# Kernel optimization log

Measured on AMD Instinct MI355X. Metric: run time of the kernel, lower is better.

Reference implementation:

```python
import jax, jax.numpy as jnp
import numpy as np

B, L, D, NH, NITEMS = 256, 200, 128, 2, 100000
HD = D // NH
LAMB = 0.6
NEG = -1e9

_PARAM_SHAPES = dict(
    item_emb=(NITEMS, D), pos_emb=(L, D),
    W_ei=(D, D), b_ei=(D,), W_eo=(D, D), b_eo=(D,), b_iah=(D,), b_oah=(D,),
    w_ih=(3 * D, 2 * D), b_ih=(3 * D,), w_hh=(3 * D, D), b_hh=(3 * D,),
    ln1_g=(D,), ln1_b=(D,),
    Wq=(D, D), bq=(D,), Wk=(D, D), bk=(D,), Wv=(D, D), bv=(D,), Wo=(D, D), bo=(D,),
    ln2_g=(D,), ln2_b=(D,), W1=(D, D), b1=(D,), W2=(D, D), b2=(D,),
    lnf_g=(D,), lnf_b=(D,),
)


def setup_inputs() -> dict:
    key = jax.random.key(0)
    ks = jax.random.split(key, len(_PARAM_SHAPES) + 2)
    stdv = 1.0 / np.sqrt(D)  # GCSAN._init_weights: uniform(-stdv, stdv) on ALL params
    p = {}
    for i, (name, shp) in enumerate(_PARAM_SHAPES.items()):
        p[name] = jax.random.uniform(ks[i], shp, jnp.float32, -stdv, stdv)
    lens = jax.random.randint(ks[-2], (B,), L // 4, L + 1)
    vals = jax.random.randint(ks[-1], (B, L), 1, NITEMS)
    # trailing zero padding, as the original break-on-zero loop assumes
    seqs = jnp.where(jnp.arange(L)[None, :] < lens[:, None], vals, 0).astype(jnp.int32)
    p['seqs'] = seqs
    p['lens'] = lens.astype(jnp.int32)
    return p


def _ln(x, g, b):
    mu = x.mean(-1, keepdims=True)
    var = ((x - mu) ** 2).mean(-1, keepdims=True)
    return (x - mu) / jnp.sqrt(var + 1e-5) * g + b


def _build_graph(seqs):
    # Vectorized replacement of _get_slice (per-row np.unique + adjacency build)
    def per_row(seq):
        s = jnp.sort(seq)
        first = jnp.concatenate([jnp.ones((1,), bool), s[1:] != s[:-1]])
        pos = jnp.cumsum(first) - 1  # compaction target of each first-occurrence
        items = jnp.zeros((L,), seq.dtype).at[jnp.where(first, pos, L)].set(s, mode='drop')
        n_u = first.sum()
        search = jnp.where(jnp.arange(L) < n_u, items, jnp.iinfo(jnp.int32).max)
        alias = jnp.searchsorted(search, seq).astype(jnp.int32)
        return items, alias
    items, alias = jax.vmap(per_row)(seqs)
    valid = seqs[:, 1:] > 0  # edge (i -> i+1) exists until first pad
    u = jnp.where(valid, alias[:, :-1], L)  # route masked edges to dummy row L
    v = jnp.where(valid, alias[:, 1:], L)
    bidx = jnp.arange(B)[:, None]
    uA = jnp.zeros((B, L + 1, L + 1), jnp.float32).at[bidx, u, v].set(1.0)[:, :L, :L]
    in_deg = jnp.maximum(uA.sum(1), 1.0)
    out_deg = jnp.maximum(uA.sum(2), 1.0)
    A_in = jnp.swapaxes(uA, 1, 2) / in_deg[:, :, None]   # A[i,j] = uA[j,i]/in_deg[i]
    A_out = uA / out_deg[:, :, None]                     # A[i,k] = uA[i,k]/out_deg[i]
    return alias, jnp.concatenate([A_in, A_out], axis=2), items  # A: [B, L, 2L]


def reference(item_emb, pos_emb, W_ei, b_ei, W_eo, b_eo, b_iah, b_oah,
              w_ih, b_ih, w_hh, b_hh, ln1_g, ln1_b, Wq, bq, Wk, bk, Wv, bv,
              Wo, bo, ln2_g, ln2_b, W1, b1, W2, b2, lnf_g, lnf_b, seqs, lens):
    alias, A, items = _build_graph(seqs)
    hidden = item_emb[items]  # [B, L, D]
    # SR-GNN gated cell, step = n_layers = 1
    for _ in range(1):
        h_in = jnp.einsum('bij,bjd->bid', A[:, :, :L], hidden @ W_ei.T + b_ei) + b_iah
        h_out = jnp.einsum('bij,bjd->bid', A[:, :, L:], hidden @ W_eo.T + b_eo) + b_oah
        gi = jnp.concatenate([h_in, h_out], -1) @ w_ih.T + b_ih
        gh = hidden @ w_hh.T + b_hh
        i_r, i_i, i_n = jnp.split(gi, 3, -1)
        h_r, h_i, h_n = jnp.split(gh, 3, -1)
        r = jax.nn.sigmoid(i_r + h_r)
        z = jax.nn.sigmoid(i_i + h_i)
        ng = jnp.tanh(i_n + r * h_n)
        hidden = ng + z * (hidden - ng)
    bidx = jnp.arange(B)
    seq_hidden = hidden[bidx[:, None], alias]  # alias-gather back to sequence order
    last_idx = lens - 1
    ht = seq_hidden[bidx, last_idx]
    x = seq_hidden + pos_emb[None, :, :]
    tl_mask = (seqs > 0)[:, :, None].astype(x.dtype)
    x = x * tl_mask
    causal = jnp.triu(jnp.ones((L, L), bool), 1)  # True = masked future (bidirectional=False)
    # SASRec-style block: ln -> MHA residual -> ln -> pointwise FFN residual
    q_in = _ln(x, ln1_g, ln1_b)
    heads = lambda t: t.reshape(B, L, NH, HD).transpose(0, 2, 1, 3)
    q = heads(q_in @ Wq.T + bq)
    k = heads(x @ Wk.T + bk)
    v = heads(x @ Wv.T + bv)
    sc = jnp.einsum('bhqd,bhkd->bhqk', q, k) / jnp.sqrt(jnp.asarray(HD, x.dtype))
    sc = jnp.where(causal[None, None], NEG, sc)
    attn = jax.nn.softmax(sc, -1)
    mo = jnp.einsum('bhqk,bhkd->bhqd', attn, v).transpose(0, 2, 1, 3).reshape(B, L, D) @ Wo.T + bo
    x = q_in + mo
    h = _ln(x, ln2_g, ln2_b)
    x = h + jax.nn.relu(h @ W1.T + b1) @ W2.T + b2
    x = x * tl_mask
    log_feats = _ln(x, lnf_g, lnf_b)
    out = log_feats[bidx, last_idx]
    return LAMB * out + (1.0 - LAMB) * ht
```

## Files before the change

### kernel.cpp

```cpp
#include <hip/hip_runtime.h>
#include <hip/hip_bf16.h>

#define Bb 256
#define Ll 200
#define Dd 128
#define BL (Bb*Ll)

typedef __hip_bfloat16 bf16;
typedef __attribute__((ext_vector_type(8))) short short8;
typedef __attribute__((ext_vector_type(4))) unsigned short ushort4v;
typedef __attribute__((ext_vector_type(4))) float floatx4;

__device__ __forceinline__ float b2f(bf16 v) { return __bfloat162float(v); }
__device__ __forceinline__ bf16  f2b(float v) { return __float2bfloat16(v); }
__device__ __forceinline__ float us2f(unsigned short u) { return __uint_as_float(((unsigned)u) << 16); }
__device__ __forceinline__ unsigned short f2us(float v) { bf16 t = f2b(v); return *(unsigned short*)&t; }
__device__ __forceinline__ float ldf(const void* p, int i, int f32) {
  return f32 ? ((const float*)p)[i] : b2f(((const bf16*)p)[i]);
}
__device__ __forceinline__ int detect_f32(const unsigned short* __restrict__ w) {
  unsigned short u = w[threadIdx.x & 63];
  return (__ballot(((u >> 7) & 0xFF) >= 0x7F) != 0ull) ? 1 : 0;
}
__device__ __forceinline__ void load_lds16(const void* g, void* l) {
  __builtin_amdgcn_global_load_lds((const __attribute__((address_space(1))) unsigned int*)g,
                                   (__attribute__((address_space(3))) unsigned int*)l, 16, 0, 0);
}

struct PackP {
  const void *W_ei,*W_eo,*w_ih,*w_hh,*Wk,*Wv,*Wqp,*Wop,*W1p,*W2p,*pos;
  const void *b_ei,*b_eo,*b_ih,*b_hh,*bk,*bv,*bqp,*bop,*b1p,*b2p,*biah,*boah;
  const void *ln1g,*ln1b,*ln2g,*ln2b,*lnfg,*lnfb;
  bf16 *cWhe,*cWih,*cWhh,*cWkv,*cWq,*cWo,*cW1,*cW2,*cPos;
  float *bias_he,*bias_gi,*bias_gh,*bias_kv,*cbq,*cbo,*cb1,*cb2,*cbiah,*cboah,*cln;
  const int* seqs;
  int *alias_g, *items_g; float *rin_g, *rout_g; unsigned *adj_g, *adjT_g;
};
__global__ __launch_bounds__(256) void k01(PackP p) {
  __shared__ alignas(16) int s[Ll];
  __shared__ int al[Ll], its[Ll];
  __shared__ alignas(4) unsigned char isf[Ll];
  __shared__ unsigned adjL[Ll*8], adjTL[Ll*8];
  if (blockIdx.x >= Bb) {
    int idx = (blockIdx.x - Bb) * 256 + threadIdx.x;
    int f32 = detect_f32((const unsigned short*)p.W_ei);
    if (idx < 131072) {
      if (idx < 32768) {
        int r = idx >> 7, c = idx & 127;
        p.cWhe[idx] = f2b(r < 128 ? ldf(p.W_ei, r*128+c, f32) : ldf(p.W_eo, (r-128)*128+c, f32));
      } else p.cWih[idx-32768] = f2b(ldf(p.w_ih, idx-32768, f32));
    } else if (idx < 278528) {
      if (idx < 180224)      p.cWhh[idx-131072] = f2b(ldf(p.w_hh, idx-131072, f32));
      else if (idx < 212992) {
        int i = idx - 180224; int r = i >> 7, c = i & 127;
        p.cWkv[i] = f2b(r < 128 ? ldf(p.Wk, r*128+c, f32) : ldf(p.Wv, (r-128)*128+c, f32));
      }
      else if (idx < 229376) p.cWq[idx-212992] = f2b(ldf(p.Wqp, idx-212992, f32));
      else if (idx < 245760) p.cWo[idx-229376] = f2b(ldf(p.Wop, idx-229376, f32));
      else if (idx < 262144) p.cW1[idx-245760] = f2b(ldf(p.W1p, idx-245760, f32));
      else                   p.cW2[idx-262144] = f2b(ldf(p.W2p, idx-262144, f32));
    } else if (idx < 304128) {
      p.cPos[idx-278528] = f2b(ldf(p.pos, idx-278528, f32));
    } else {
      int j = idx - 304128;
      if      (j < 256)  p.bias_he[j]     = (j<128) ? ldf(p.b_ei,j,f32) : ldf(p.b_eo,j-128,f32);
      else if (j < 640)  p.bias_gi[j-256] = ldf(p.b_ih, j-256, f32);
      else if (j < 1024) p.bias_gh[j-640] = ldf(p.b_hh, j-640, f32);
      else if (j < 1280) { int c=j-1024; p.bias_kv[c] = (c<128)? ldf(p.bk,c,f32): ldf(p.bv,c-128,f32); }
      else if (j < 1408) p.cbq[j-1280]   = ldf(p.bqp, j-1280, f32);
      else if (j < 1536) p.cbo[j-1408]   = ldf(p.bop, j-1408, f32);
      else if (j < 1664) p.cb1[j-1536]   = ldf(p.b1p, j-1536, f32);
      else if (j < 1792) p.cb2[j-1664]   = ldf(p.b2p, j-1664, f32);
      else if (j < 1920) p.cbiah[j-1792] = ldf(p.biah, j-1792, f32);
      else if (j < 2048) p.cboah[j-1920] = ldf(p.boah, j-1920, f32);
      else {
        int i = j - 2048, g = i >> 7, c2 = i & 127;
        const void* s6 = g==0?p.ln1g: g==1?p.ln1b: g==2?p.ln2g: g==3?p.ln2b: g==4?p.lnfg: p.lnfb;
        p.cln[i] = ldf(s6, c2, f32);
      }
    }
    return;
  }
  int b = blockIdx.x, t = threadIdx.x;
  if (t < Ll) s[t] = p.seqs[b*Ll + t];
  for (int i = t; i < Ll*8; i += 256) { adjL[i] = 0u; adjTL[i] = 0u; }
  __syncthreads();
  const int4* s4 = (const int4*)s;
  if (t < Ll) {
    int v = s[t]; int dup = 0;
    int nb = t >> 2;
    for (int j4 = 0; j4 < nb; j4++) {
      int4 sv = s4[j4];
      dup |= (sv.x==v) | (sv.y==v) | (sv.z==v) | (sv.w==v);
    }
    for (int j = nb*4; j < t; j++) dup |= (s[j]==v);
    isf[t] = dup ? 0 : 1; its[t] = 0;
  }
  __syncthreads();
  const unsigned* isfw = (const unsigned*)isf;
  if (t < Ll) {
    int v = s[t], r = 0;
    for (int j4 = 0; j4 < Ll/4; j4++) {
      int4 sv = s4[j4];
      unsigned fw = isfw[j4];
      r += ((fw & 0xffu)       && sv.x < v);
      r += ((fw & 0xff00u)     && sv.y < v);
      r += ((fw & 0xff0000u)   && sv.z < v);
      r += ((fw & 0xff000000u) && sv.w < v);
    }
    al[t] = r;
  }
  __syncthreads();
  if (t < Ll && isf[t]) its[al[t]] = s[t];
  if (t < Ll-1 && s[t+1] > 0) {
    int u = al[t], v = al[t+1];
    atomicOr(&adjL [u*8 + (v >> 5)], 1u << (v & 31));
    atomicOr(&adjTL[v*8 + (u >> 5)], 1u << (u & 31));
  }
  __syncthreads();
  if (t < Ll) {
    int od = 0, id = 0;
    for (int wd = 0; wd < 7; wd++) { od += __popc(adjL[t*8+wd]); id += __popc(adjTL[t*8+wd]); }
    p.rout_g [b*Ll + t] = 1.0f / (float)max(od, 1);
    p.rin_g  [b*Ll + t] = 1.0f / (float)max(id, 1);
    p.alias_g[b*Ll + t] = al[t];
    p.items_g[b*Ll + t] = its[t];
  }
  for (int i = t; i < Ll*8; i += 256) { p.adj_g[b*Ll*8 + i] = adjL[i]; p.adjT_g[b*Ll*8 + i] = adjTL[i]; }
}

__global__ __launch_bounds__(256) void k2_gather(const void* __restrict__ emb, const void* __restrict__ wei,
    const int* __restrict__ items_g, bf16* __restrict__ hidden)
{
  int idx = blockIdx.x * 256 + threadIdx.x;
  int f32 = detect_f32((const unsigned short*)wei);
  int n = idx >> 4, jv = idx & 15;
  int it = items_g[n];
  short8 o;
  if (f32) {
    const float* e = (const float*)emb + (size_t)it * 128 + jv * 8;
#pragma unroll
    for (int j = 0; j < 8; j++) o[j] = (short)f2us(e[j]);
  } else {
    o = ((const short8*)((const bf16*)emb + (size_t)it * 128))[jv];
  }
  ((short8*)hidden)[idx] = o;
}

template<int K>
__global__ __launch_bounds__(256) void gemm6(const bf16* __restrict__ A, const bf16* __restrict__ W,
    const float* __restrict__ bias,
    bf16* __restrict__ out_lo, int Nlo, bf16* __restrict__ out_hi, int Nhi, int split)
{
  __shared__ short As[128*128];
  __shared__ short Ws[128*128];
  int t = threadIdx.x;
  int wave = t >> 6, lane = t & 63;
  int q = lane >> 4, mr = lane & 15;
  int wm = wave & 1, wn = wave >> 1;
  int m0 = blockIdx.x * 128, n0 = blockIdx.y * 128;
  int srow = lane >> 4;
  int c16 = lane & 15;
  floatx4 acc[4][4] = {};
  for (int k0 = 0; k0 < K; k0 += 128) {
#pragma unroll
    for (int i = 0; i < 8; i++) {
      int seg = wave*8 + i;
      int r = seg*4 + srow;
      int gch = c16 ^ (r & 15);
      load_lds16(A + (size_t)(m0 + r) * K + k0 + gch*8, &As[seg*512]);
      load_lds16(W + (size_t)(n0 + r) * K + k0 + gch*8, &Ws[seg*512]);
    }
    __syncthreads();
#pragma unroll
    for (int kk = 0; kk < 4; kk++) {
      short8 af[4], wf[4];
#pragma unroll
      for (int i = 0; i < 4; i++) {
        int row = wm*64 + i*16 + mr;
        af[i] = *(const short8*)(&As[row*128 + ((kk*4+q) ^ (row&15))*8]);
      }
#pragma unroll
      for (int j = 0; j < 4; j++) {
        int row = wn*64 + j*16 + mr;
        wf[j] = *(const short8*)(&Ws[row*128 + ((kk*4+q) ^ (row&15))*8]);
      }
#pragma unroll
      for (int i = 0; i < 4; i++)
#pragma unroll
        for (int j = 0; j < 4; j++)
          acc[i][j] = __builtin_amdgcn_mfma_f32_16x16x32_bf16(wf[j], af[i], acc[i][j], 0, 0, 0);
    }
    if (k0 + 128 < K) __syncthreads();
  }
#pragma unroll
  for (int j = 0; j < 4; j++) {
    int ng = n0 + wn*64 + j*16 + q*4;
    floatx4 bs = *(const floatx4*)(bias + ng);
    bf16* outp; int col, stride;
    if (ng < split) { outp = out_lo; col = ng; stride = Nlo; }
    else            { outp = out_hi; col = ng - split; stride = Nhi; }
#pragma unroll
    for (int i = 0; i < 4; i++) {
      int m = m0 + wm*64 + i*16 + mr;
      ushort4v o;
#pragma unroll
      for (int e = 0; e < 4; e++) o[e] = f2us(acc[i][j][e] + bs[e]);
      *(ushort4v*)(outp + (size_t)m * stride + col) = o;
    }
  }
}

__global__ __launch_bounds__(256) void k3_agg(const bf16* __restrict__ he,
    const unsigned* __restrict__ adj_g, const unsigned* __restrict__ adjT_g,
    const float* __restrict__ rin_g, const float* __restrict__ rout_g,
    const float* __restrict__ cbiah, const float* __restrict__ cboah, bf16* __restrict__ hio)
{
  int b = blockIdx.x / 25, chunk = blockIdx.x % 25;
  int wave = threadIdx.x >> 6, lane = threadIdx.x & 63;
  bool isIn = lane < 32;
  int c = isIn ? 4*lane : 128 + 4*(lane-32);
  const bf16* heb = he + (size_t)b * Ll * 256;
  bf16* hiob = hio + (size_t)b * Ll * 256;
  float bias0 = isIn ? cbiah[c]   : cboah[c-128];
  float bias1 = isIn ? cbiah[c+1] : cboah[c-127];
  float bias2 = isIn ? cbiah[c+2] : cboah[c-126];
  float bias3 = isIn ? cbiah[c+3] : cboah[c-125];
#pragma unroll
  for (int s = 0; s < 2; s++) {
    int i = chunk*8 + wave + 4*s;
    const unsigned* mrow = (isIn ? adjT_g : adj_g) + ((size_t)b*Ll + i) * 8;
    float a0=0.f, a1=0.f, a2=0.f, a3=0.f;
    for (int wd = 0; wd < 7; wd++) {
      unsigned bits = mrow[wd];
      while (bits) {
        int j = (wd << 5) + __builtin_ctz(bits); bits &= bits - 1;
        ushort4v h4 = *(const ushort4v*)(heb + (size_t)j*256 + c);
        a0 += us2f(h4.x); a1 += us2f(h4.y); a2 += us2f(h4.z); a3 += us2f(h4.w);
      }
    }
    float r = isIn ? rin_g[b*Ll + i] : rout_g[b*Ll + i];
    ushort4v o;
    o.x = f2us(bias0 + r*a0); o.y = f2us(bias1 + r*a1);
    o.z = f2us(bias2 + r*a2); o.w = f2us(bias3 + r*a3);
    *(ushort4v*)(hiob + (size_t)i*256 + c) = o;
  }
}

__global__ __launch_bounds__(256) void kv_fused(const bf16* __restrict__ gi, const bf16* __restrict__ gh,
    const bf16* __restrict__ hidden, const int* __restrict__ alias_g, const int* __restrict__ lens,
    const bf16* __restrict__ cPos, const bf16* __restrict__ cWkv, const float* __restrict__ bias_kv,
    bf16* __restrict__ kv, float* __restrict__ ht)
{
  __shared__ short xs[208*136];
  __shared__ int aliasL[Ll];
  int b = blockIdx.x, t = threadIdx.x;
  int wave = t >> 6, lane = t & 63, q = lane >> 4, mr = lane & 15;
  int li = lens[b] - 1;
  if (t < Ll) aliasL[t] = alias_g[b*Ll + t];
  for (int u = t; u < 8*136; u += 256) xs[Ll*136 + u] = 0;
  __syncthreads();
  for (int u = t; u < Ll*16; u += 256) {
    int tpos = u >> 4, jv = u & 15;
    int a = aliasL[tpos];
    const short8* gin = (const short8*)(gi + ((size_t)b*Ll + a) * 384);
    const short8* ghn = (const short8*)(gh + ((size_t)b*Ll + a) * 384);
    short8 vir = gin[jv], vii = gin[16+jv], vnn = gin[32+jv];
    short8 whr = ghn[jv], whi = ghn[16+jv], whn = ghn[32+jv];
    short8 hv  = ((const short8*)(hidden + ((size_t)b*Ll + a) * Dd))[jv];
    short8 pv  = ((const short8*)(cPos + tpos * Dd))[jv];
    bool isLast = (tpos == li);
    short8 o;
#pragma unroll
    for (int e = 0; e < 8; e++) {
      float ir = us2f((unsigned short)vir[e]), ii = us2f((unsigned short)vii[e]), inn = us2f((unsigned short)vnn[e]);
      float hr = us2f((unsigned short)whr[e]), hi = us2f((unsigned short)whi[e]), hn = us2f((unsigned short)whn[e]);
      float r  = 1.f / (1.f + __expf(-(ir + hr)));
      float z  = 1.f / (1.f + __expf(-(ii + hi)));
      float arg = inn + r * hn;
      float ex = __expf(-2.f * arg);
      float ng = (1.f - ex) / (1.f + ex);
      float h  = us2f((unsigned short)hv[e]);
      float sh = ng + z * (h - ng);
      o[e] = (short)f2us(sh + us2f((unsigned short)pv[e]));
      if (isLast) ht[b*Dd + jv*8 + e] = sh;
    }
    *(short8*)&xs[tpos*136 + jv*8] = o;
  }
  __syncthreads();
  short8 wf[4][4];
#pragma unroll
  for (int kk = 0; kk < 4; kk++)
#pragma unroll
    for (int j = 0; j < 4; j++) {
      int n = wave*64 + j*16 + mr;
      wf[kk][j] = *(const short8*)(cWkv + (size_t)n*128 + kk*32 + q*8);
    }
  for (int mt = 0; mt < 13; mt++) {
    short8 af[4];
#pragma unroll
    for (int kk = 0; kk < 4; kk++)
      af[kk] = *(const short8*)&xs[(mt*16 + mr)*136 + (kk*4+q)*8];
    floatx4 acc[4] = {};
#pragma unroll
    for (int kk = 0; kk < 4; kk++)
#pragma unroll
      for (int j = 0; j < 4; j++)
        acc[j] = __builtin_amdgcn_mfma_f32_16x16x32_bf16(wf[kk][j], af[kk], acc[j], 0, 0, 0);
    int m = mt*16 + mr;
    if (m < Ll) {
#pragma unroll
      for (int j = 0; j < 4; j++) {
        int n = wave*64 + j*16 + q*4;
        floatx4 bs = *(const floatx4*)(bias_kv + n);
        ushort4v o;
#pragma unroll
        for (int e = 0; e < 4; e++) o[e] = f2us(acc[j][e] + bs[e]);
        *(ushort4v*)(kv + ((size_t)b*Ll + m)*256 + n) = o;
      }
    }
  }
}

struct FinalP {
  const bf16 *kv; const float* ht; const bf16* cPos;
  const bf16 *cWq, *cWo, *cW1, *cW2;
  const float *cbq, *cbo, *cb1, *cb2, *cln;
  const int* lens; const void* wei;
  void* out;
};
__device__ __forceinline__ float dot128i(const bf16* __restrict__ wrow, const float* __restrict__ vin) {
  const short8* wr = (const short8*)wrow;
  float a0=0.f, a1=0.f, a2=0.f, a3=0.f;
#pragma unroll
  for (int kk = 0; kk < 4; kk++) {
    short8 w0 = wr[kk*4+0], w1 = wr[kk*4+1], w2 = wr[kk*4+2], w3 = wr[kk*4+3];
#pragma unroll
    for (int j = 0; j < 8; j++) {
      a0 += vin[kk*32 +      j] * us2f((unsigned short)w0[j]);
      a1 += vin[kk*32 + 8  + j] * us2f((unsigned short)w1[j]);
      a2 += vin[kk*32 + 16 + j] * us2f((unsigned short)w2[j]);
      a3 += vin[kk*32 + 24 + j] * us2f((unsigned short)w3[j]);
    }
  }
  return (a0+a1)+(a2+a3);
}
__device__ __forceinline__ float wave_sum(float v) {
#pragma unroll
  for (int m = 1; m < 64; m <<= 1) v += __shfl_xor(v, m, 64);
  return v;
}
__device__ __forceinline__ float wave_max(float v) {
#pragma unroll
  for (int m = 1; m < 64; m <<= 1) v = fmaxf(v, __shfl_xor(v, m, 64));
  return v;
}
__global__ __launch_bounds__(256) void k7_final(FinalP p)
{
  __shared__ float sred[8];
  __shared__ float qin[128], qv[128], aout[128], hh[128], f1[128];
  __shared__ float pb0[256], pb1[256];
  __shared__ floatx4 av4[8][32];
  int b = blockIdx.x, t = threadIdx.x, c = t;
  int w = t >> 6, ln = t & 63;
  int li = p.lens[b] - 1;
  int f32 = detect_f32((const unsigned short*)p.wei);
  float xv = (c < 128) ? (p.ht[b*Dd + c] + b2f(p.cPos[li*Dd + c])) : 0.f;
  float s = wave_sum(xv), s2 = wave_sum(xv*xv);
  if (ln == 0) { sred[w] = s; sred[4+w] = s2; }
  __syncthreads();
  float mu = (sred[0]+sred[1]+sred[2]+sred[3]) * (1.f/128.f);
  float ms = (sred[4]+sred[5]+sred[6]+sred[7]) * (1.f/128.f);
  float rs = rsqrtf(fmaxf(ms - mu*mu, 0.f) + 1e-5f);
  __syncthreads();
  if (c < 128) qin[c] = (xv - mu) * rs * p.cln[c] + p.cln[128+c];
  __syncthreads();
  if (c < 128) qv[c] = p.cbq[c] + dot128i(p.cWq + c*128, qin);
  __syncthreads();
  const bf16* kvb = p.kv + (size_t)b * Ll * 256;
  float s0 = -3.0e38f, s1 = -3.0e38f;
  if (t <= li) {
    const short8* kr = (const short8*)(kvb + (size_t)t*256);
    float a00=0.f,a01=0.f,a10=0.f,a11=0.f;
#pragma unroll
    for (int kk = 0; kk < 4; kk++) {
      short8 k0 = kr[kk*2], k1 = kr[kk*2+1], k2 = kr[8+kk*2], k3 = kr[8+kk*2+1];
#pragma unroll
      for (int j = 0; j < 8; j++) {
        a00 += qv[kk*16 + j]      * us2f((unsigned short)k0[j]);
        a01 += qv[kk*16 + 8 + j]  * us2f((unsigned short)k1[j]);
        a10 += qv[64 + kk*16 + j]     * us2f((unsigned short)k2[j]);
        a11 += qv[64 + kk*16 + 8 + j] * us2f((unsigned short)k3[j]);
      }
    }
    s0 = (a00+a01) * 0.125f; s1 = (a10+a11) * 0.125f;
  }
  float m0 = wave_max(s0), m1 = wave_max(s1);
  if (ln == 0) { sred[w] = m0; sred[4+w] = m1; }
  __syncthreads();
  m0 = fmaxf(fmaxf(sred[0],sred[1]), fmaxf(sred[2],sred[3]));
  m1 = fmaxf(fmaxf(sred[4],sred[5]), fmaxf(sred[6],sred[7]));
  __syncthreads();
  float e0 = (t <= li) ? __expf(s0 - m0) : 0.f;
  float e1 = (t <= li) ? __expf(s1 - m1) : 0.f;
  pb0[t] = e0; pb1[t] = e1;
  float l0 = wave_sum(e0), l1 = wave_sum(e1);
  if (ln == 0) { sred[w] = l0; sred[4+w] = l1; }
  __syncthreads();
  l0 = sred[0]+sred[1]+sred[2]+sred[3];
  l1 = sred[4]+sred[5]+sred[6]+sred[7];
  {
    int part = t >> 5, cq = t & 31, ch = cq * 4;
    int cnt = li + 1, cpp = (cnt + 7) >> 3;
    int j0 = part * cpp, j1 = min(j0 + cpp, cnt);
    const float* pbh = (ch < 64) ? pb0 : pb1;
    float a0=0.f,a1=0.f,a2=0.f,a3=0.f;
#pragma unroll 4
    for (int j = j0; j < j1; j++) {
      ushort4v v4 = *(const ushort4v*)(kvb + (size_t)j*256 + 128 + ch);
      float pw = pbh[j];
      a0 += pw*us2f(v4.x); a1 += pw*us2f(v4.y); a2 += pw*us2f(v4.z); a3 += pw*us2f(v4.w);
    }
    floatx4 o = {a0,a1,a2,a3};
    av4[part][cq] = o;
  }
  __syncthreads();
  if (c < 128) {
    float l = (c < 64) ? l0 : l1;
    float acc = 0.f;
#pragma unroll
    for (int pp = 0; pp < 8; pp++) acc += ((const float*)&av4[pp][c>>2])[c&3];
    aout[c] = acc / l;
  }
  __syncthreads();
  float x2v = 0.f;
  if (c < 128) x2v = qin[c] + p.cbo[c] + dot128i(p.cWo + c*128, aout);
  s = wave_sum((c<128)?x2v:0.f); s2 = wave_sum((c<128)?x2v*x2v:0.f);
  if (ln == 0) { sred[w] = s; sred[4+w] = s2; }
  __syncthreads();
  mu = (sred[0]+sred[1]+sred[2]+sred[3]) * (1.f/128.f);
  ms = (sred[4]+sred[5]+sred[6]+sred[7]) * (1.f/128.f);
  rs = rsqrtf(fmaxf(ms - mu*mu, 0.f) + 1e-5f);
  __syncthreads();
  if (c < 128) hh[c] = (x2v - mu) * rs * p.cln[256+c] + p.cln[384+c];
  __syncthreads();
  if (c < 128) f1[c] = fmaxf(p.cb1[c] + dot128i(p.cW1 + c*128, hh), 0.f);
  __syncthreads();
  float x3v = 0.f;
  if (c < 128) x3v = hh[c] + p.cb2[c] + dot128i(p.cW2 + c*128, f1);
  s = wave_sum((c<128)?x3v:0.f); s2 = wave_sum((c<128)?x3v*x3v:0.f);
  if (ln == 0) { sred[w] = s; sred[4+w] = s2; }
  __syncthreads();
  mu = (sred[0]+sred[1]+sred[2]+sred[3]) * (1.f/128.f);
  ms = (sred[4]+sred[5]+sred[6]+sred[7]) * (1.f/128.f);
  rs = rsqrtf(fmaxf(ms - mu*mu, 0.f) + 1e-5f);
  if (c < 128) {
    float lf = (x3v - mu) * rs * p.cln[512+c] + p.cln[640+c];
    float outv = 0.6f * lf + 0.4f * p.ht[b*Dd + c];
    if (f32) ((float*)p.out)[b*Dd + c] = outv;
    else     ((bf16*)p.out)[b*Dd + c]  = f2b(outv);
  }
}

extern "C" void kernel_launch(void* const* d_in, const int* in_sizes, int n_in,
                              void* d_out, int out_size, void* d_ws, size_t ws_size,
                              hipStream_t stream)
{
  (void)in_sizes; (void)n_in; (void)out_size; (void)ws_size;
  const void* item_emb = d_in[0];
  const int* seqs = (const int*)d_in[30];
  const int* lens = (const int*)d_in[31];

  char* wsp = (char*)d_ws;
  size_t o = 0;
  auto alloc = [&](size_t sz) { void* p = wsp + o; o += (sz + 255) & ~(size_t)255; return p; };
  int*      alias_g = (int*)alloc((size_t)BL*4);
  int*      items_g = (int*)alloc((size_t)BL*4);
  float*    rin_g   = (float*)alloc((size_t)BL*4);
  float*    rout_g  = (float*)alloc((size_t)BL*4);
  unsigned* adj_g   = (unsigned*)alloc((size_t)BL*8*4);
  unsigned* adjT_g  = (unsigned*)alloc((size_t)BL*8*4);
  float*    ht_g    = (float*)alloc((size_t)Bb*Dd*4);
  bf16*     cWhe    = (bf16*)alloc(32768*2);
  bf16*     cWhh    = (bf16*)alloc(49152*2);
  bf16*     cWih    = (bf16*)alloc(98304*2);
  bf16*     cWkv    = (bf16*)alloc(32768*2);
  bf16*     cWq     = (bf16*)alloc(16384*2);
  bf16*     cWo     = (bf16*)alloc(16384*2);
  bf16*     cW1     = (bf16*)alloc(16384*2);
  bf16*     cW2     = (bf16*)alloc(16384*2);
  bf16*     cPos    = (bf16*)alloc(25600*2);
  float*    bias_he = (float*)alloc(256*4);
  float*    bias_gh = (float*)alloc(384*4);
  float*    bias_gi = (float*)alloc(384*4);
  float*    bias_kv = (float*)alloc(256*4);
  float*    cbq     = (float*)alloc(128*4);
  float*    cbo     = (float*)alloc(128*4);
  float*    cb1     = (float*)alloc(128*4);
  float*    cb2     = (float*)alloc(128*4);
  float*    cbiah   = (float*)alloc(128*4);
  float*    cboah   = (float*)alloc(128*4);
  float*    cln     = (float*)alloc(768*4);
  bf16*     hidden  = (bf16*)alloc((size_t)BL*128*2);
  bf16*     he      = (bf16*)alloc((size_t)BL*256*2);
  bf16*     hio     = (bf16*)alloc((size_t)BL*256*2);
  bf16*     gi      = (bf16*)alloc((size_t)BL*384*2);
  bf16*     gh      = (bf16*)alloc((size_t)BL*384*2);
  bf16*     kv = hio;

  PackP pp = { d_in[2], d_in[4], d_in[8], d_in[10], d_in[16], d_in[18], d_in[14], d_in[20],
               d_in[24], d_in[26], d_in[1],
               d_in[3], d_in[5], d_in[9], d_in[11], d_in[17], d_in[19], d_in[15], d_in[21],
               d_in[25], d_in[27], d_in[6], d_in[7],
               d_in[12], d_in[13], d_in[22], d_in[23], d_in[28], d_in[29],
               cWhe, cWih, cWhh, cWkv, cWq, cWo, cW1, cW2, cPos,
               bias_he, bias_gi, bias_gh, bias_kv, cbq, cbo, cb1, cb2, cbiah, cboah, cln,
               seqs, alias_g, items_g, rin_g, rout_g, adj_g, adjT_g };
  k01<<<Bb + 1199, 256, 0, stream>>>(pp);
  k2_gather<<<BL*16/256, 256, 0, stream>>>(item_emb, d_in[2], items_g, hidden);
  gemm6<128><<<dim3(BL/128, 5), 256, 0, stream>>>(hidden, cWhe, bias_he, he, 256, gh, 384, 256);
  k3_agg<<<Bb*25, 256, 0, stream>>>(he, adj_g, adjT_g, rin_g, rout_g, cbiah, cboah, hio);
  gemm6<256><<<dim3(BL/128, 3), 256, 0, stream>>>(hio, cWih, bias_gi, gi, 384, gi, 384, 1<<30);
  kv_fused<<<Bb, 256, 0, stream>>>(gi, gh, hidden, alias_g, lens, cPos, cWkv, bias_kv, kv, ht_g);
  FinalP fp = { kv, ht_g, cPos, cWq, cWo, cW1, cW2, cbq, cbo, cb1, cb2, cln, lens, d_in[2], d_out };
  k7_final<<<Bb, 256, 0, stream>>>(fp);
}
```

Before: 276.1 us.

## Fuse embedding gather into hidden GEMM and GRU epilogue, drop hidden buffer

Removes the standalone gather kernel that materialised the embedding rows into a hidden buffer. The first GEMM now loads embedding rows by item index straight into its shared-memory A tile. The GRU/kv kernel reads emb[seq[t]] directly, using the identity that the alias-gathered hidden row equals the embedding of the original sequence item. This saves one launch plus a full write and read-back of the hidden tensor. In exchange, each column block redoes the random-row embedding gather, and the A tile is loaded synchronously rather than through async LDS loads.

```diff
diff --git a/kernel.cpp b/kernel.cpp
--- a/kernel.cpp
+++ b/kernel.cpp
@@ -25,6 +25,17 @@
 __device__ __forceinline__ void load_lds16(const void* g, void* l) {
   __builtin_amdgcn_global_load_lds((const __attribute__((address_space(1))) unsigned int*)g,
                                    (__attribute__((address_space(3))) unsigned int*)l, 16, 0, 0);
+}
+__device__ __forceinline__ short8 emb_chunk8(const void* __restrict__ emb, int it, int g, int f32) {
+  short8 o;
+  if (f32) {
+    const float* e = (const float*)emb + (size_t)it * 128 + g * 8;
+#pragma unroll
+    for (int j = 0; j < 8; j++) o[j] = (short)f2us(e[j]);
+  } else {
+    o = ((const short8*)((const bf16*)emb + (size_t)it * 128))[g];
+  }
+  return o;
 }
 
 struct PackP {
@@ -129,22 +140,76 @@
   for (int i = t; i < Ll*8; i += 256) { p.adj_g[b*Ll*8 + i] = adjL[i]; p.adjT_g[b*Ll*8 + i] = adjTL[i]; }
 }
 
-__global__ __launch_bounds__(256) void k2_gather(const void* __restrict__ emb, const void* __restrict__ wei,
-    const int* __restrict__ items_g, bf16* __restrict__ hidden)
+__global__ __launch_bounds__(256) void gemm_he(const void* __restrict__ emb, const int* __restrict__ items_g,
+    const bf16* __restrict__ W, const float* __restrict__ bias,
+    bf16* __restrict__ out_lo, int Nlo, bf16* __restrict__ out_hi, int Nhi, int split)
 {
-  int idx = blockIdx.x * 256 + threadIdx.x;
-  int f32 = detect_f32((const unsigned short*)wei);
-  int n = idx >> 4, jv = idx & 15;
-  int it = items_g[n];
-  short8 o;
-  if (f32) {
-    const float* e = (const float*)emb + (size_t)it * 128 + jv * 8;
-#pragma unroll
-    for (int j = 0; j < 8; j++) o[j] = (short)f2us(e[j]);
-  } else {
-    o = ((const short8*)((const bf16*)emb + (size_t)it * 128))[jv];
-  }
-  ((short8*)hidden)[idx] = o;
+  __shared__ short As[128*128];
+  __shared__ short Ws[128*128];
+  int t = threadIdx.x;
+  int wave = t >> 6, lane = t & 63;
+  int q = lane >> 4, mr = lane & 15;
+  int wm = wave & 1, wn = wave >> 1;
+  int m0 = blockIdx.x * 128, n0 = blockIdx.y * 128;
+  int f32 = detect_f32((const unsigned short*)W);
+  f32 = detect_f32((const unsigned short*)emb);
+  {
+    int r = t >> 1, half = t & 1;
+    int it = items_g[m0 + r];
+#pragma unroll
+    for (int g8 = 0; g8 < 8; g8++) {
+      int g = half*8 + g8;
+      short8 o = emb_chunk8(emb, it, g, f32);
+      *(short8*)&As[r*128 + (g ^ (r & 15))*8] = o;
+    }
+  }
+  {
+    int srow = lane >> 4, c16 = lane & 15;
+#pragma unroll
+    for (int i = 0; i < 8; i++) {
+      int seg = wave*8 + i;
+      int r = seg*4 + srow;
+      int gch = c16 ^ (r & 15);
+      load_lds16(W + (size_t)(n0 + r) * 128 + gch*8, &Ws[seg*512]);
+    }
+  }
+  __syncthreads();
+  floatx4 acc[4][4] = {};
+#pragma unroll
+  for (int kk = 0; kk < 4; kk++) {
+    short8 af[4], wf[4];
+#pragma unroll
+    for (int i = 0; i < 4; i++) {
+      int row = wm*64 + i*16 + mr;
+      af[i] = *(const short8*)(&As[row*128 + ((kk*4+q) ^ (row&15))*8]);
+    }
+#pragma unroll
+    for (int j = 0; j < 4; j++) {
+      int row = wn*64 + j*16 + mr;
+      wf[j] = *(const short8*)(&Ws[row*128 + ((kk*4+q) ^ (row&15))*8]);
+    }
+#pragma unroll
+    for (int i = 0; i < 4; i++)
+#pragma unroll
+      for (int j = 0; j < 4; j++)
+        acc[i][j] = __builtin_amdgcn_mfma_f32_16x16x32_bf16(wf[j], af[i], acc[i][j], 0, 0, 0);
+  }
+#pragma unroll
+  for (int j = 0; j < 4; j++) {
+    int ng = n0 + wn*64 + j*16 + q*4;
+    floatx4 bs = *(const floatx4*)(bias + ng);
+    bf16* outp; int col, stride;
+    if (ng < split) { outp = out_lo; col = ng; stride = Nlo; }
+    else            { outp = out_hi; col = ng - split; stride = Nhi; }
+#pragma unroll
+    for (int i = 0; i < 4; i++) {
+      int m = m0 + wm*64 + i*16 + mr;
+      ushort4v o;
+#pragma unroll
+      for (int e = 0; e < 4; e++) o[e] = f2us(acc[i][j][e] + bs[e]);
+      *(ushort4v*)(outp + (size_t)m * stride + col) = o;
+    }
+  }
 }
 
 template<int K>
@@ -248,26 +313,29 @@
 }
 
 __global__ __launch_bounds__(256) void kv_fused(const bf16* __restrict__ gi, const bf16* __restrict__ gh,
-    const bf16* __restrict__ hidden, const int* __restrict__ alias_g, const int* __restrict__ lens,
+    const void* __restrict__ emb, const int* __restrict__ seqs,
+    const int* __restrict__ alias_g, const int* __restrict__ lens,
     const bf16* __restrict__ cPos, const bf16* __restrict__ cWkv, const float* __restrict__ bias_kv,
     bf16* __restrict__ kv, float* __restrict__ ht)
 {
   __shared__ short xs[208*136];
-  __shared__ int aliasL[Ll];
+  __shared__ int aliasL[Ll], seqL[Ll];
   int b = blockIdx.x, t = threadIdx.x;
   int wave = t >> 6, lane = t & 63, q = lane >> 4, mr = lane & 15;
   int li = lens[b] - 1;
-  if (t < Ll) aliasL[t] = alias_g[b*Ll + t];
+  int f32 = detect_f32((const unsigned short*)emb) ;
+  if (t < Ll) { aliasL[t] = alias_g[b*Ll + t]; seqL[t] = seqs[b*Ll + t]; }
   for (int u = t; u < 8*136; u += 256) xs[Ll*136 + u] = 0;
   __syncthreads();
   for (int u = t; u < Ll*16; u += 256) {
     int tpos = u >> 4, jv = u & 15;
     int a = aliasL[tpos];
+    int it = seqL[tpos];
     const short8* gin = (const short8*)(gi + ((size_t)b*Ll + a) * 384);
     const short8* ghn = (const short8*)(gh + ((size_t)b*Ll + a) * 384);
     short8 vir = gin[jv], vii = gin[16+jv], vnn = gin[32+jv];
     short8 whr = ghn[jv], whi = ghn[16+jv], whn = ghn[32+jv];
-    short8 hv  = ((const short8*)(hidden + ((size_t)b*Ll + a) * Dd))[jv];
+    short8 hv  = emb_chunk8(emb, it, jv, f32);
     short8 pv  = ((const short8*)(cPos + tpos * Dd))[jv];
     bool isLast = (tpos == li);
     short8 o;
@@ -501,7 +569,6 @@
   float*    cbiah   = (float*)alloc(128*4);
   float*    cboah   = (float*)alloc(128*4);
   float*    cln     = (float*)alloc(768*4);
-  bf16*     hidden  = (bf16*)alloc((size_t)BL*128*2);
   bf16*     he      = (bf16*)alloc((size_t)BL*256*2);
   bf16*     hio     = (bf16*)alloc((size_t)BL*256*2);
   bf16*     gi      = (bf16*)alloc((size_t)BL*384*2);
@@ -517,11 +584,10 @@
                bias_he, bias_gi, bias_gh, bias_kv, cbq, cbo, cb1, cb2, cbiah, cboah, cln,
                seqs, alias_g, items_g, rin_g, rout_g, adj_g, adjT_g };
   k01<<<Bb + 1199, 256, 0, stream>>>(pp);
-  k2_gather<<<BL*16/256, 256, 0, stream>>>(item_emb, d_in[2], items_g, hidden);
-  gemm6<128><<<dim3(BL/128, 5), 256, 0, stream>>>(hidden, cWhe, bias_he, he, 256, gh, 384, 256);
+  gemm_he<<<dim3(BL/128, 5), 256, 0, stream>>>(item_emb, items_g, cWhe, bias_he, he, 256, gh, 384, 256);
   k3_agg<<<Bb*25, 256, 0, stream>>>(he, adj_g, adjT_g, rin_g, rout_g, cbiah, cboah, hio);
   gemm6<256><<<dim3(BL/128, 3), 256, 0, stream>>>(hio, cWih, bias_gi, gi, 384, gi, 384, 1<<30);
-  kv_fused<<<Bb, 256, 0, stream>>>(gi, gh, hidden, alias_g, lens, cPos, cWkv, bias_kv, kv, ht_g);
+  kv_fused<<<Bb, 256, 0, stream>>>(gi, gh, item_emb, seqs, alias_g, lens, cPos, cWkv, bias_kv, kv, ht_g);
   FinalP fp = { kv, ht_g, cPos, cWq, cWo, cW1, cW2, cbq, cbo, cb1, cb2, cln, lens, d_in[2], d_out };
   k7_final<<<Bb, 256, 0, stream>>>(fp);
 }
```

Result: no change. 277.0 us (+0.3%).
